# Kernel tuning notes

Hardware: AMD Instinct MI355X
Metric: run time of the kernel (lower is better)

The kernel has to match this reference:

```python
import jax, jax.numpy as jnp
import numpy as np

H_PARAM = 3.0   # filtering strength h
TWS = 5         # template window size
SWS = 11        # search window size


def _shift_stack(x, window_size):
    # [N,C,H,W] -> [N,C,H,W,window_size**2] of circularly shifted copies.
    # Shift order matches the torch module: outer loop x_shift, inner y_shift,
    # roll shifts=(y_shift, x_shift) on dims (H, W).
    r = window_size // 2
    return jnp.stack(
        [jnp.roll(x, (ys, xs), axis=(2, 3))
         for xs in range(-r, r + 1) for ys in range(-r, r + 1)],
        axis=-1,
    )


def _box_filter(x, window_size):
    # Circular box-sum over H,W dims. The torch double roll loop is separable,
    # so do it as two 1-D roll sums (10 rolls instead of 25 for tws=5).
    r = window_size // 2
    s = x
    acc = x
    for k in range(1, r + 1):
        acc = acc + jnp.roll(s, k, axis=3) + jnp.roll(s, -k, axis=3)
    s2 = acc
    for k in range(1, r + 1):
        acc = acc + jnp.roll(s2, k, axis=2) + jnp.roll(s2, -k, axis=2)
    return acc


def setup_inputs() -> dict:
    key = jax.random.key(0)
    x = jax.random.uniform(key, (2, 3, 512, 512), dtype=jnp.float32)
    return {"x": x}


def reference(x):
    # luminance (RGB input: C == 3)
    xc = jnp.clip(x, 0.0, 1.0)
    y = 0.299 * xc[:, :1] + 0.587 * xc[:, 1:2] + 0.114 * xc[:, 2:3]  # [N,1,H,W]

    x_stack = _shift_stack(x, SWS)  # [N,3,H,W,sws^2]
    y_stack = _shift_stack(y, SWS)  # [N,1,H,W,sws^2]

    d2 = _box_filter((y[..., None] - y_stack) ** 2, TWS)  # [N,1,H,W,sws^2]
    distances = jnp.sqrt(d2)
    weights = jnp.exp(-distances / H_PARAM)                # [N,1,H,W,sws^2]

    denoised = (weights * x_stack).sum(axis=-1) / weights.sum(axis=-1)
    return jnp.clip(denoised, 0.0, 1.0)
```

## Files before the change

kernel.cpp:

```cpp
#include <hip/hip_runtime.h>
#include <math.h>


#define H_IMG 512
#define W_IMG 512
#define MASK  511
#define HWSZ  (H_IMG * W_IMG)
#define TILE  32
#define HALO  7
#define XD    46
#define YSTR  48
#define HSTR  44
#define VSTR  44

typedef _Float16 h2 __attribute__((ext_vector_type(2)));

__device__ __forceinline__ float fdot2(h2 a, h2 b, float c) {
#if __has_builtin(__builtin_amdgcn_fdot2)
    return __builtin_amdgcn_fdot2(a, b, c, false);
#else
    return c + (float)a.x * (float)b.x + (float)a.y * (float)b.y;
#endif
}

__device__ __forceinline__ float fast_exp2(float x) {
#if __has_builtin(__builtin_amdgcn_exp2f)
    return __builtin_amdgcn_exp2f(x);
#else
    return __expf(x * 0.6931471805599453f);
#endif
}

#define K2C   0.23126321070979063f
#define N2K2 -0.46252642141958126f

__global__ __launch_bounds__(256, 4)
void nlm_kernel(const float* __restrict__ x, float* __restrict__ out) {
    __shared__ float4   ldsX[XD * XD];
    __shared__ float    ldsYf[XD * YSTR];
    __shared__ unsigned ldsY2[XD * YSTR];
    __shared__ float    ldsH[XD * HSTR];
    __shared__ float    ldsV[42 * VSTR];

    const int n  = blockIdx.z;
    const int ti = blockIdx.y * TILE;
    const int tj = blockIdx.x * TILE;
    const int tx = threadIdx.x;
    const int ty = threadIdx.y;
    const int tid = ty * 32 + tx;

    const float* xb = x + (size_t)n * 3 * HWSZ;

    for (int e = tid; e < XD * XD; e += 256) {
        int r = e / XD, c = e - r * XD;
        int gi = (ti + r - HALO) & MASK;
        int gj = (tj + c - HALO) & MASK;
        size_t o = (size_t)gi * W_IMG + gj;
        ldsX[e] = make_float4(xb[o], xb[o + HWSZ], xb[o + 2 * HWSZ], 0.f);
    }
    __syncthreads();

    for (int e = tid; e < XD * 47; e += 256) {
        int r = e / 47, c = e - r * 47;
        int cs = (c == 46) ? 45 : c;
        float4 v = ldsX[r * XD + cs];
        float rr = fminf(fmaxf(v.x, 0.f), 1.f);
        float gg = fminf(fmaxf(v.y, 0.f), 1.f);
        float bb = fminf(fmaxf(v.z, 0.f), 1.f);
        ldsYf[r * YSTR + c] = 0.299f * rr + 0.587f * gg + 0.114f * bb;
    }
    __syncthreads();

    for (int e = tid; e < XD * XD; e += 256) {
        int r = e / XD, c = e - r * XD;
        h2 p;
        p.x = (_Float16)ldsYf[r * YSTR + c];
        p.y = (_Float16)ldsYf[r * YSTR + c + 1];
        ldsY2[r * YSTR + c] = __builtin_bit_cast(unsigned, p);
    }
    __syncthreads();

    for (int e = tid; e < XD * 42; e += 256) {
        int r = e / 42, c = e - r * 42;
        h2 a  = __builtin_bit_cast(h2, ldsY2[r * YSTR + c]);
        h2 b  = __builtin_bit_cast(h2, ldsY2[r * YSTR + c + 2]);
        h2 cc = __builtin_bit_cast(h2, ldsY2[r * YSTR + c + 4]);
        float x0 = (float)a.x, x1 = (float)a.y;
        float x2 = (float)b.x, x3 = (float)b.y;
        float x4 = (float)cc.x;
        ldsH[r * HSTR + c] = x0*x0 + x1*x1 + x2*x2 + x3*x3 + x4*x4;
    }
    __syncthreads();

    for (int e = tid; e < 42 * 42; e += 256) {
        int r = e / 42, c = e - r * 42;
        const float* hp = &ldsH[r * HSTR + c];
        float s = ((hp[0] + hp[HSTR]) + (hp[2*HSTR] + hp[3*HSTR])) + hp[4*HSTR];
        ldsV[r * VSTR + c] = K2C * s;
    }
    __syncthreads();

    const int jl = tx + HALO;
    const int il = ty * 4 + HALO;

    h2 cyP[8][3];
    float Vc[4];
    {
        float hcv[8];
        #pragma unroll
        for (int t = 0; t < 8; ++t) {
            int base = (il - 2 + t) * YSTR + (jl - 2);
            cyP[t][0] = __builtin_bit_cast(h2, ldsY2[base]);
            cyP[t][1] = __builtin_bit_cast(h2, ldsY2[base + 2]);
            h2 z = __builtin_bit_cast(h2, ldsY2[base + 4]);
            z.y = (_Float16)0.f;
            cyP[t][2] = z;
            hcv[t] = ldsH[(il - 2 + t) * HSTR + (jl - 2)];
        }
        float v0 = ((hcv[0] + hcv[1]) + (hcv[2] + hcv[3])) + hcv[4];
        float v1 = v0 - hcv[0] + hcv[5];
        float v2 = v1 - hcv[1] + hcv[6];
        float v3 = v2 - hcv[2] + hcv[7];
        Vc[0] = K2C * v0; Vc[1] = K2C * v1; Vc[2] = K2C * v2; Vc[3] = K2C * v3;
    }

    float den[4]  = {0.f, 0.f, 0.f, 0.f};
    float num0[4] = {0.f, 0.f, 0.f, 0.f};
    float num1[4] = {0.f, 0.f, 0.f, 0.f};
    float num2[4] = {0.f, 0.f, 0.f, 0.f};

    #pragma unroll 1
    for (int xs = -5; xs <= 5; ++xs) {
        const int jc  = jl - xs - 2;
        const int xjc = jl - xs;

        h2     swP[8][3];
        float  Wr[4];
        float4 xw[4];

        #pragma unroll
        for (int t = 0; t < 8; ++t) {
            int base = (il - 7 + t) * YSTR + jc;
            swP[t][0] = __builtin_bit_cast(h2, ldsY2[base]);
            swP[t][1] = __builtin_bit_cast(h2, ldsY2[base + 2]);
            swP[t][2] = __builtin_bit_cast(h2, ldsY2[base + 4]);
        }
        #pragma unroll
        for (int t = 0; t < 4; ++t) {
            Wr[t] = ldsV[(il - 7 + t) * VSTR + jc];
            xw[t] = ldsX[(il - 5 + t) * XD + xjc];
        }

        #pragma unroll
        for (int k = 0; k <= 10; ++k) {
            h2 nsw0, nsw1, nsw2; float nWv; float4 nxw;
            if (k < 10) {
                const int nr = il + k + 1;
                int base = nr * YSTR + jc;
                nsw0 = __builtin_bit_cast(h2, ldsY2[base]);
                nsw1 = __builtin_bit_cast(h2, ldsY2[base + 2]);
                nsw2 = __builtin_bit_cast(h2, ldsY2[base + 4]);
                nWv  = ldsV[(il + k - 3) * VSTR + jc];
                nxw  = ldsX[(il + k - 1) * XD + xjc];
            }

            float s[8];
            #pragma unroll
            for (int t = 0; t < 8; ++t) {
                const int m = (t + k) & 7;
                s[t] = fdot2(cyP[t][0], swP[m][0],
                       fdot2(cyP[t][1], swP[m][1],
                       fdot2(cyP[t][2], swP[m][2], 0.f)));
            }

            float S0 = ((s[0] + s[1]) + (s[2] + s[3])) + s[4];
            float S1 = S0 - s[0] + s[5];
            float S2 = S1 - s[1] + s[6];
            float S3 = S2 - s[2] + s[7];

            float d2a[4];
            d2a[0] = fmaf(N2K2, S0, Vc[0] + Wr[k & 3]);
            d2a[1] = fmaf(N2K2, S1, Vc[1] + Wr[(k + 1) & 3]);
            d2a[2] = fmaf(N2K2, S2, Vc[2] + Wr[(k + 2) & 3]);
            d2a[3] = fmaf(N2K2, S3, Vc[3] + Wr[(k + 3) & 3]);

            #pragma unroll
            for (int o = 0; o < 4; ++o) {
                float sd = __builtin_amdgcn_sqrtf(__builtin_fabsf(d2a[o]));
                float w  = fast_exp2(-sd);
                float4 xv = xw[(k + o) & 3];
                num0[o] = fmaf(w, xv.x, num0[o]);
                num1[o] = fmaf(w, xv.y, num1[o]);
                num2[o] = fmaf(w, xv.z, num2[o]);
                den[o] += w;
            }

            if (k < 10) {
                swP[k & 7][0] = nsw0;
                swP[k & 7][1] = nsw1;
                swP[k & 7][2] = nsw2;
                Wr[k & 3] = nWv;
                xw[k & 3] = nxw;
            }
        }
    }

    float* ob = out + (size_t)n * 3 * HWSZ;
    #pragma unroll
    for (int o = 0; o < 4; ++o) {
        int gi = ti + ty * 4 + o;
        int gj = tj + tx;
        size_t off = (size_t)gi * W_IMG + gj;
        float inv = __builtin_amdgcn_rcpf(den[o]);
        float v0 = fminf(fmaxf(num0[o] * inv, 0.f), 1.f);
        float v1 = fminf(fmaxf(num1[o] * inv, 0.f), 1.f);
        float v2 = fminf(fmaxf(num2[o] * inv, 0.f), 1.f);
        ob[off]            = v0;
        ob[off + HWSZ]     = v1;
        ob[off + 2 * HWSZ] = v2;
    }
}

extern "C" void kernel_launch(void* const* d_in, const int* in_sizes, int n_in,
                              void* d_out, int out_size, void* d_ws, size_t ws_size,
                              hipStream_t stream) {
    const float* x = (const float*)d_in[0];
    float* out = (float*)d_out;
    dim3 grid(W_IMG / TILE, H_IMG / TILE, 2);
    dim3 block(32, 8);
    nlm_kernel<<<grid, block, 0, stream>>>(x, out);
}
```

Measured before the change: 98.98 us.

## Double threads per tile, each computing two output rows instead of four

Raises the block to 512 threads (32x16) and cuts each thread's register-blocked strip from four rows to two, shrinking the sliding window of template rows from 8 to 6. Centre V values now come from the precomputed ldsV table. The aim is more parallelism per tile and lower register pressure. The cost is less reuse of the sliding window: each thread handles 6 template rows for 2 outputs instead of 8 for 4, so dot-product work and LDS loads per output pixel go up.

```diff
diff --git a/kernel.cpp b/kernel.cpp
--- a/kernel.cpp
+++ b/kernel.cpp
@@ -12,6 +12,7 @@
 #define YSTR  48
 #define HSTR  44
 #define VSTR  44
+#define NTHR  512
 
 typedef _Float16 h2 __attribute__((ext_vector_type(2)));
 
@@ -34,7 +35,7 @@
 #define K2C   0.23126321070979063f
 #define N2K2 -0.46252642141958126f
 
-__global__ __launch_bounds__(256, 4)
+__global__ __launch_bounds__(NTHR, 4)
 void nlm_kernel(const float* __restrict__ x, float* __restrict__ out) {
     __shared__ float4   ldsX[XD * XD];
     __shared__ float    ldsYf[XD * YSTR];
@@ -51,7 +52,7 @@
 
     const float* xb = x + (size_t)n * 3 * HWSZ;
 
-    for (int e = tid; e < XD * XD; e += 256) {
+    for (int e = tid; e < XD * XD; e += NTHR) {
         int r = e / XD, c = e - r * XD;
         int gi = (ti + r - HALO) & MASK;
         int gj = (tj + c - HALO) & MASK;
@@ -60,7 +61,7 @@
     }
     __syncthreads();
 
-    for (int e = tid; e < XD * 47; e += 256) {
+    for (int e = tid; e < XD * 47; e += NTHR) {
         int r = e / 47, c = e - r * 47;
         int cs = (c == 46) ? 45 : c;
         float4 v = ldsX[r * XD + cs];
@@ -71,7 +72,7 @@
     }
     __syncthreads();
 
-    for (int e = tid; e < XD * XD; e += 256) {
+    for (int e = tid; e < XD * XD; e += NTHR) {
         int r = e / XD, c = e - r * XD;
         h2 p;
         p.x = (_Float16)ldsYf[r * YSTR + c];
@@ -80,7 +81,7 @@
     }
     __syncthreads();
 
-    for (int e = tid; e < XD * 42; e += 256) {
+    for (int e = tid; e < XD * 42; e += NTHR) {
         int r = e / 42, c = e - r * 42;
         h2 a  = __builtin_bit_cast(h2, ldsY2[r * YSTR + c]);
         h2 b  = __builtin_bit_cast(h2, ldsY2[r * YSTR + c + 2]);
@@ -92,7 +93,7 @@
     }
     __syncthreads();
 
-    for (int e = tid; e < 42 * 42; e += 256) {
+    for (int e = tid; e < 42 * 42; e += NTHR) {
         int r = e / 42, c = e - r * 42;
         const float* hp = &ldsH[r * HSTR + c];
         float s = ((hp[0] + hp[HSTR]) + (hp[2*HSTR] + hp[3*HSTR])) + hp[4*HSTR];
@@ -101,73 +102,64 @@
     __syncthreads();
 
     const int jl = tx + HALO;
-    const int il = ty * 4 + HALO;
-
-    h2 cyP[8][3];
-    float Vc[4];
-    {
-        float hcv[8];
-        #pragma unroll
-        for (int t = 0; t < 8; ++t) {
-            int base = (il - 2 + t) * YSTR + (jl - 2);
-            cyP[t][0] = __builtin_bit_cast(h2, ldsY2[base]);
-            cyP[t][1] = __builtin_bit_cast(h2, ldsY2[base + 2]);
-            h2 z = __builtin_bit_cast(h2, ldsY2[base + 4]);
-            z.y = (_Float16)0.f;
-            cyP[t][2] = z;
-            hcv[t] = ldsH[(il - 2 + t) * HSTR + (jl - 2)];
-        }
-        float v0 = ((hcv[0] + hcv[1]) + (hcv[2] + hcv[3])) + hcv[4];
-        float v1 = v0 - hcv[0] + hcv[5];
-        float v2 = v1 - hcv[1] + hcv[6];
-        float v3 = v2 - hcv[2] + hcv[7];
-        Vc[0] = K2C * v0; Vc[1] = K2C * v1; Vc[2] = K2C * v2; Vc[3] = K2C * v3;
-    }
-
-    float den[4]  = {0.f, 0.f, 0.f, 0.f};
-    float num0[4] = {0.f, 0.f, 0.f, 0.f};
-    float num1[4] = {0.f, 0.f, 0.f, 0.f};
-    float num2[4] = {0.f, 0.f, 0.f, 0.f};
+    const int il = ty * 2 + HALO;
+
+    h2 cyP[6][3];
+    float Vc[2];
+    #pragma unroll
+    for (int t = 0; t < 6; ++t) {
+        int base = (il - 2 + t) * YSTR + (jl - 2);
+        cyP[t][0] = __builtin_bit_cast(h2, ldsY2[base]);
+        cyP[t][1] = __builtin_bit_cast(h2, ldsY2[base + 2]);
+        h2 z = __builtin_bit_cast(h2, ldsY2[base + 4]);
+        z.y = (_Float16)0.f;
+        cyP[t][2] = z;
+    }
+    Vc[0] = ldsV[(il - 2) * VSTR + (jl - 2)];
+    Vc[1] = ldsV[(il - 1) * VSTR + (jl - 2)];
+
+    float den[2]  = {0.f, 0.f};
+    float num0[2] = {0.f, 0.f};
+    float num1[2] = {0.f, 0.f};
+    float num2[2] = {0.f, 0.f};
 
     #pragma unroll 1
     for (int xs = -5; xs <= 5; ++xs) {
         const int jc  = jl - xs - 2;
         const int xjc = jl - xs;
 
-        h2     swP[8][3];
-        float  Wr[4];
-        float4 xw[4];
+        h2     swP[6][3];
+        float  Wr[2];
+        float4 xw[2];
 
         #pragma unroll
-        for (int t = 0; t < 8; ++t) {
+        for (int t = 0; t < 6; ++t) {
             int base = (il - 7 + t) * YSTR + jc;
             swP[t][0] = __builtin_bit_cast(h2, ldsY2[base]);
             swP[t][1] = __builtin_bit_cast(h2, ldsY2[base + 2]);
             swP[t][2] = __builtin_bit_cast(h2, ldsY2[base + 4]);
         }
-        #pragma unroll
-        for (int t = 0; t < 4; ++t) {
-            Wr[t] = ldsV[(il - 7 + t) * VSTR + jc];
-            xw[t] = ldsX[(il - 5 + t) * XD + xjc];
-        }
+        Wr[0] = ldsV[(il - 7) * VSTR + jc];
+        Wr[1] = ldsV[(il - 6) * VSTR + jc];
+        xw[0] = ldsX[(il - 5) * XD + xjc];
+        xw[1] = ldsX[(il - 4) * XD + xjc];
 
         #pragma unroll
         for (int k = 0; k <= 10; ++k) {
             h2 nsw0, nsw1, nsw2; float nWv; float4 nxw;
             if (k < 10) {
-                const int nr = il + k + 1;
-                int base = nr * YSTR + jc;
+                int base = (il + k - 1) * YSTR + jc;
                 nsw0 = __builtin_bit_cast(h2, ldsY2[base]);
                 nsw1 = __builtin_bit_cast(h2, ldsY2[base + 2]);
                 nsw2 = __builtin_bit_cast(h2, ldsY2[base + 4]);
-                nWv  = ldsV[(il + k - 3) * VSTR + jc];
-                nxw  = ldsX[(il + k - 1) * XD + xjc];
-            }
-
-            float s[8];
+                nWv  = ldsV[(il + k - 5) * VSTR + jc];
+                nxw  = ldsX[(il + k - 3) * XD + xjc];
+            }
+
+            float s[6];
             #pragma unroll
-            for (int t = 0; t < 8; ++t) {
-                const int m = (t + k) & 7;
+            for (int t = 0; t < 6; ++t) {
+                const int m = (t + k) % 6;
                 s[t] = fdot2(cyP[t][0], swP[m][0],
                        fdot2(cyP[t][1], swP[m][1],
                        fdot2(cyP[t][2], swP[m][2], 0.f)));
@@ -175,40 +167,43 @@
 
             float S0 = ((s[0] + s[1]) + (s[2] + s[3])) + s[4];
             float S1 = S0 - s[0] + s[5];
-            float S2 = S1 - s[1] + s[6];
-            float S3 = S2 - s[2] + s[7];
-
-            float d2a[4];
-            d2a[0] = fmaf(N2K2, S0, Vc[0] + Wr[k & 3]);
-            d2a[1] = fmaf(N2K2, S1, Vc[1] + Wr[(k + 1) & 3]);
-            d2a[2] = fmaf(N2K2, S2, Vc[2] + Wr[(k + 2) & 3]);
-            d2a[3] = fmaf(N2K2, S3, Vc[3] + Wr[(k + 3) & 3]);
-
-            #pragma unroll
-            for (int o = 0; o < 4; ++o) {
-                float sd = __builtin_amdgcn_sqrtf(__builtin_fabsf(d2a[o]));
+
+            float d2a0 = fmaf(N2K2, S0, Vc[0] + Wr[k & 1]);
+            float d2a1 = fmaf(N2K2, S1, Vc[1] + Wr[(k + 1) & 1]);
+
+            {
+                float sd = __builtin_amdgcn_sqrtf(__builtin_fabsf(d2a0));
                 float w  = fast_exp2(-sd);
-                float4 xv = xw[(k + o) & 3];
-                num0[o] = fmaf(w, xv.x, num0[o]);
-                num1[o] = fmaf(w, xv.y, num1[o]);
-                num2[o] = fmaf(w, xv.z, num2[o]);
-                den[o] += w;
+                float4 xv = xw[k & 1];
+                num0[0] = fmaf(w, xv.x, num0[0]);
+                num1[0] = fmaf(w, xv.y, num1[0]);
+                num2[0] = fmaf(w, xv.z, num2[0]);
+                den[0] += w;
+            }
+            {
+                float sd = __builtin_amdgcn_sqrtf(__builtin_fabsf(d2a1));
+                float w  = fast_exp2(-sd);
+                float4 xv = xw[(k + 1) & 1];
+                num0[1] = fmaf(w, xv.x, num0[1]);
+                num1[1] = fmaf(w, xv.y, num1[1]);
+                num2[1] = fmaf(w, xv.z, num2[1]);
+                den[1] += w;
             }
 
             if (k < 10) {
-                swP[k & 7][0] = nsw0;
-                swP[k & 7][1] = nsw1;
-                swP[k & 7][2] = nsw2;
-                Wr[k & 3] = nWv;
-                xw[k & 3] = nxw;
+                swP[k % 6][0] = nsw0;
+                swP[k % 6][1] = nsw1;
+                swP[k % 6][2] = nsw2;
+                Wr[k & 1] = nWv;
+                xw[k & 1] = nxw;
             }
         }
     }
 
     float* ob = out + (size_t)n * 3 * HWSZ;
     #pragma unroll
-    for (int o = 0; o < 4; ++o) {
-        int gi = ti + ty * 4 + o;
+    for (int o = 0; o < 2; ++o) {
+        int gi = ti + ty * 2 + o;
         int gj = tj + tx;
         size_t off = (size_t)gi * W_IMG + gj;
         float inv = __builtin_amdgcn_rcpf(den[o]);
@@ -227,6 +222,6 @@
     const float* x = (const float*)d_in[0];
     float* out = (float*)d_out;
     dim3 grid(W_IMG / TILE, H_IMG / TILE, 2);
-    dim3 block(32, 8);
+    dim3 block(32, 16);
     nlm_kernel<<<grid, block, 0, stream>>>(x, out);
 }
```

After: 105.3 us. +6.4%, slower.

## Software-pipeline weight evaluation, pack FMA accumulators, read center V from LDS

Applied to the files above, without the earlier changes.

The sqrt/exp weight computation and the accumulation for each row are deferred by one iteration of the inner k loop, so the transcendental work overlaps with the next row's dot products and LDS loads. The first two color accumulators are packed into a float2 so the compiler can emit packed FMA. The center-window V terms are now read directly from the precomputed ldsV instead of being rebuilt from ldsH. Launch bounds drop from 4 to 2 blocks per SM, which gives the extra pipelined live values more registers but may reduce occupancy.

```diff
diff --git a/kernel.cpp b/kernel.cpp
--- a/kernel.cpp
+++ b/kernel.cpp
@@ -14,6 +14,7 @@
 #define VSTR  44
 
 typedef _Float16 h2 __attribute__((ext_vector_type(2)));
+typedef float f32x2 __attribute__((ext_vector_type(2)));
 
 __device__ __forceinline__ float fdot2(h2 a, h2 b, float c) {
 #if __has_builtin(__builtin_amdgcn_fdot2)
@@ -34,7 +35,7 @@
 #define K2C   0.23126321070979063f
 #define N2K2 -0.46252642141958126f
 
-__global__ __launch_bounds__(256, 4)
+__global__ __launch_bounds__(256, 2)
 void nlm_kernel(const float* __restrict__ x, float* __restrict__ out) {
     __shared__ float4   ldsX[XD * XD];
     __shared__ float    ldsYf[XD * YSTR];
@@ -105,29 +106,26 @@
 
     h2 cyP[8][3];
     float Vc[4];
-    {
-        float hcv[8];
-        #pragma unroll
-        for (int t = 0; t < 8; ++t) {
-            int base = (il - 2 + t) * YSTR + (jl - 2);
-            cyP[t][0] = __builtin_bit_cast(h2, ldsY2[base]);
-            cyP[t][1] = __builtin_bit_cast(h2, ldsY2[base + 2]);
-            h2 z = __builtin_bit_cast(h2, ldsY2[base + 4]);
-            z.y = (_Float16)0.f;
-            cyP[t][2] = z;
-            hcv[t] = ldsH[(il - 2 + t) * HSTR + (jl - 2)];
-        }
-        float v0 = ((hcv[0] + hcv[1]) + (hcv[2] + hcv[3])) + hcv[4];
-        float v1 = v0 - hcv[0] + hcv[5];
-        float v2 = v1 - hcv[1] + hcv[6];
-        float v3 = v2 - hcv[2] + hcv[7];
-        Vc[0] = K2C * v0; Vc[1] = K2C * v1; Vc[2] = K2C * v2; Vc[3] = K2C * v3;
-    }
-
-    float den[4]  = {0.f, 0.f, 0.f, 0.f};
-    float num0[4] = {0.f, 0.f, 0.f, 0.f};
-    float num1[4] = {0.f, 0.f, 0.f, 0.f};
-    float num2[4] = {0.f, 0.f, 0.f, 0.f};
+    #pragma unroll
+    for (int t = 0; t < 8; ++t) {
+        int base = (il - 2 + t) * YSTR + (jl - 2);
+        cyP[t][0] = __builtin_bit_cast(h2, ldsY2[base]);
+        cyP[t][1] = __builtin_bit_cast(h2, ldsY2[base + 2]);
+        h2 z = __builtin_bit_cast(h2, ldsY2[base + 4]);
+        z.y = (_Float16)0.f;
+        cyP[t][2] = z;
+    }
+    #pragma unroll
+    for (int o = 0; o < 4; ++o)
+        Vc[o] = ldsV[(il - 2 + o) * VSTR + (jl - 2)];
+
+    f32x2 acc01[4];
+    float num2[4], den[4];
+    #pragma unroll
+    for (int o = 0; o < 4; ++o) {
+        acc01[o] = (f32x2){0.f, 0.f};
+        num2[o] = 0.f; den[o] = 0.f;
+    }
 
     #pragma unroll 1
     for (int xs = -5; xs <= 5; ++xs) {
@@ -150,6 +148,9 @@
             Wr[t] = ldsV[(il - 7 + t) * VSTR + jc];
             xw[t] = ldsX[(il - 5 + t) * XD + xjc];
         }
+
+        float  pd2[4];
+        float4 pxv;
 
         #pragma unroll
         for (int k = 0; k <= 10; ++k) {
@@ -184,18 +185,24 @@
             d2a[2] = fmaf(N2K2, S2, Vc[2] + Wr[(k + 2) & 3]);
             d2a[3] = fmaf(N2K2, S3, Vc[3] + Wr[(k + 3) & 3]);
 
+            if (k > 0) {
+                #pragma unroll
+                for (int o = 0; o < 4; ++o) {
+                    float4 xv = (o == 0) ? pxv : xw[(k - 1 + o) & 3];
+                    float sd = __builtin_amdgcn_sqrtf(__builtin_fabsf(pd2[o]));
+                    float w  = fast_exp2(-sd);
+                    f32x2 bw = {w, w};
+                    f32x2 xv01 = {xv.x, xv.y};
+                    acc01[o] = __builtin_elementwise_fma(bw, xv01, acc01[o]);
+                    num2[o] = fmaf(w, xv.z, num2[o]);
+                    den[o] += w;
+                }
+            }
+
             #pragma unroll
-            for (int o = 0; o < 4; ++o) {
-                float sd = __builtin_amdgcn_sqrtf(__builtin_fabsf(d2a[o]));
-                float w  = fast_exp2(-sd);
-                float4 xv = xw[(k + o) & 3];
-                num0[o] = fmaf(w, xv.x, num0[o]);
-                num1[o] = fmaf(w, xv.y, num1[o]);
-                num2[o] = fmaf(w, xv.z, num2[o]);
-                den[o] += w;
-            }
-
+            for (int o = 0; o < 4; ++o) pd2[o] = d2a[o];
             if (k < 10) {
+                pxv = xw[k & 3];
                 swP[k & 7][0] = nsw0;
                 swP[k & 7][1] = nsw1;
                 swP[k & 7][2] = nsw2;
@@ -203,6 +210,18 @@
                 xw[k & 3] = nxw;
             }
         }
+
+        #pragma unroll
+        for (int o = 0; o < 4; ++o) {
+            float4 xv = xw[(10 + o) & 3];
+            float sd = __builtin_amdgcn_sqrtf(__builtin_fabsf(pd2[o]));
+            float w  = fast_exp2(-sd);
+            f32x2 bw = {w, w};
+            f32x2 xv01 = {xv.x, xv.y};
+            acc01[o] = __builtin_elementwise_fma(bw, xv01, acc01[o]);
+            num2[o] = fmaf(w, xv.z, num2[o]);
+            den[o] += w;
+        }
     }
 
     float* ob = out + (size_t)n * 3 * HWSZ;
@@ -212,9 +231,9 @@
         int gj = tj + tx;
         size_t off = (size_t)gi * W_IMG + gj;
         float inv = __builtin_amdgcn_rcpf(den[o]);
-        float v0 = fminf(fmaxf(num0[o] * inv, 0.f), 1.f);
-        float v1 = fminf(fmaxf(num1[o] * inv, 0.f), 1.f);
-        float v2 = fminf(fmaxf(num2[o] * inv, 0.f), 1.f);
+        float v0 = fminf(fmaxf(acc01[o].x * inv, 0.f), 1.f);
+        float v1 = fminf(fmaxf(acc01[o].y * inv, 0.f), 1.f);
+        float v2 = fminf(fmaxf(num2[o]   * inv, 0.f), 1.f);
         ob[off]            = v0;
         ob[off + HWSZ]     = v1;
         ob[off + 2 * HWSZ] = v2;
```

After: 98.42 us. No clear change (-0.6%).

## Process two horizontal shifts per iteration and trade occupancy for ILP

Applied to the files above, without the earlier changes.

Restructures the 11-step horizontal shift loop into one single-shift group followed by five groups that each handle two shifts, interleaving their dot products and exp/sqrt chains to expose more instruction-level parallelism. Launch bounds drop from 4 to 2 waves per SIMD hint so the doubled register state fits. Vc is now read from the precomputed ldsV instead of being recomputed from ldsH. The risk is lower occupancy and register pressure or spills in exchange for fewer loop-carried dependencies.

```diff
diff --git a/kernel.cpp b/kernel.cpp
--- a/kernel.cpp
+++ b/kernel.cpp
@@ -34,7 +34,104 @@
 #define K2C   0.23126321070979063f
 #define N2K2 -0.46252642141958126f
 
-__global__ __launch_bounds__(256, 4)
+template <int NU>
+__device__ __forceinline__ void nlm_xs_group(
+    int xs0, int jl, int il,
+    const unsigned* __restrict__ ldsY2,
+    const float*    __restrict__ ldsV,
+    const float4*   __restrict__ ldsX,
+    const h2 (&cyP)[8][3], const float (&Vc)[4],
+    float (&num0)[4], float (&num1)[4], float (&num2)[4], float (&den)[4])
+{
+    h2     swP[NU][8][3];
+    float  Wr[NU][4];
+    float4 xw[NU][4];
+    int    jc[NU], xjc[NU];
+
+    #pragma unroll
+    for (int u = 0; u < NU; ++u) {
+        const int xs = xs0 + u;
+        jc[u]  = jl - xs - 2;
+        xjc[u] = jl - xs;
+        #pragma unroll
+        for (int t = 0; t < 8; ++t) {
+            int base = (il - 7 + t) * YSTR + jc[u];
+            swP[u][t][0] = __builtin_bit_cast(h2, ldsY2[base]);
+            swP[u][t][1] = __builtin_bit_cast(h2, ldsY2[base + 2]);
+            swP[u][t][2] = __builtin_bit_cast(h2, ldsY2[base + 4]);
+        }
+        #pragma unroll
+        for (int t = 0; t < 4; ++t) {
+            Wr[u][t] = ldsV[(il - 7 + t) * VSTR + jc[u]];
+            xw[u][t] = ldsX[(il - 5 + t) * XD + xjc[u]];
+        }
+    }
+
+    #pragma unroll
+    for (int k = 0; k <= 10; ++k) {
+        h2 nsw[NU][3]; float nWv[NU]; float4 nxw[NU];
+        if (k < 10) {
+            #pragma unroll
+            for (int u = 0; u < NU; ++u) {
+                int base = (il + k + 1) * YSTR + jc[u];
+                nsw[u][0] = __builtin_bit_cast(h2, ldsY2[base]);
+                nsw[u][1] = __builtin_bit_cast(h2, ldsY2[base + 2]);
+                nsw[u][2] = __builtin_bit_cast(h2, ldsY2[base + 4]);
+                nWv[u] = ldsV[(il + k - 3) * VSTR + jc[u]];
+                nxw[u] = ldsX[(il + k - 1) * XD + xjc[u]];
+            }
+        }
+
+        float s[NU][8];
+        #pragma unroll
+        for (int t = 0; t < 8; ++t) {
+            const int m = (t + k) & 7;
+            #pragma unroll
+            for (int u = 0; u < NU; ++u)
+                s[u][t] = fdot2(cyP[t][0], swP[u][m][0],
+                          fdot2(cyP[t][1], swP[u][m][1],
+                          fdot2(cyP[t][2], swP[u][m][2], 0.f)));
+        }
+
+        #pragma unroll
+        for (int u = 0; u < NU; ++u) {
+            float S0 = ((s[u][0] + s[u][1]) + (s[u][2] + s[u][3])) + s[u][4];
+            float S1 = S0 - s[u][0] + s[u][5];
+            float S2 = S1 - s[u][1] + s[u][6];
+            float S3 = S2 - s[u][2] + s[u][7];
+
+            float d2a[4];
+            d2a[0] = fmaf(N2K2, S0, Vc[0] + Wr[u][k & 3]);
+            d2a[1] = fmaf(N2K2, S1, Vc[1] + Wr[u][(k + 1) & 3]);
+            d2a[2] = fmaf(N2K2, S2, Vc[2] + Wr[u][(k + 2) & 3]);
+            d2a[3] = fmaf(N2K2, S3, Vc[3] + Wr[u][(k + 3) & 3]);
+
+            #pragma unroll
+            for (int o = 0; o < 4; ++o) {
+                float sd = __builtin_amdgcn_sqrtf(__builtin_fabsf(d2a[o]));
+                float w  = fast_exp2(-sd);
+                float4 xv = xw[u][(k + o) & 3];
+                num0[o] = fmaf(w, xv.x, num0[o]);
+                num1[o] = fmaf(w, xv.y, num1[o]);
+                num2[o] = fmaf(w, xv.z, num2[o]);
+                den[o] += w;
+            }
+        }
+
+        if (k < 10) {
+            #pragma unroll
+            for (int u = 0; u < NU; ++u) {
+                swP[u][k & 7][0] = nsw[u][0];
+                swP[u][k & 7][1] = nsw[u][1];
+                swP[u][k & 7][2] = nsw[u][2];
+                Wr[u][k & 3] = nWv[u];
+                xw[u][k & 3] = nxw[u];
+            }
+        }
+    }
+}
+
+__global__ __launch_bounds__(256, 2)
 void nlm_kernel(const float* __restrict__ x, float* __restrict__ out) {
     __shared__ float4   ldsX[XD * XD];
     __shared__ float    ldsYf[XD * YSTR];
@@ -105,105 +202,30 @@
 
     h2 cyP[8][3];
     float Vc[4];
-    {
-        float hcv[8];
-        #pragma unroll
-        for (int t = 0; t < 8; ++t) {
-            int base = (il - 2 + t) * YSTR + (jl - 2);
-            cyP[t][0] = __builtin_bit_cast(h2, ldsY2[base]);
-            cyP[t][1] = __builtin_bit_cast(h2, ldsY2[base + 2]);
-            h2 z = __builtin_bit_cast(h2, ldsY2[base + 4]);
-            z.y = (_Float16)0.f;
-            cyP[t][2] = z;
-            hcv[t] = ldsH[(il - 2 + t) * HSTR + (jl - 2)];
-        }
-        float v0 = ((hcv[0] + hcv[1]) + (hcv[2] + hcv[3])) + hcv[4];
-        float v1 = v0 - hcv[0] + hcv[5];
-        float v2 = v1 - hcv[1] + hcv[6];
-        float v3 = v2 - hcv[2] + hcv[7];
-        Vc[0] = K2C * v0; Vc[1] = K2C * v1; Vc[2] = K2C * v2; Vc[3] = K2C * v3;
-    }
-
-    float den[4]  = {0.f, 0.f, 0.f, 0.f};
+    #pragma unroll
+    for (int t = 0; t < 8; ++t) {
+        int base = (il - 2 + t) * YSTR + (jl - 2);
+        cyP[t][0] = __builtin_bit_cast(h2, ldsY2[base]);
+        cyP[t][1] = __builtin_bit_cast(h2, ldsY2[base + 2]);
+        h2 z = __builtin_bit_cast(h2, ldsY2[base + 4]);
+        z.y = (_Float16)0.f;
+        cyP[t][2] = z;
+    }
+    #pragma unroll
+    for (int o = 0; o < 4; ++o)
+        Vc[o] = ldsV[(il - 2 + o) * VSTR + (jl - 2)];
+
     float num0[4] = {0.f, 0.f, 0.f, 0.f};
     float num1[4] = {0.f, 0.f, 0.f, 0.f};
     float num2[4] = {0.f, 0.f, 0.f, 0.f};
-
+    float den[4]  = {0.f, 0.f, 0.f, 0.f};
+
+    nlm_xs_group<1>(-5, jl, il, ldsY2, ldsV, ldsX, cyP, Vc,
+                    num0, num1, num2, den);
     #pragma unroll 1
-    for (int xs = -5; xs <= 5; ++xs) {
-        const int jc  = jl - xs - 2;
-        const int xjc = jl - xs;
-
-        h2     swP[8][3];
-        float  Wr[4];
-        float4 xw[4];
-
-        #pragma unroll
-        for (int t = 0; t < 8; ++t) {
-            int base = (il - 7 + t) * YSTR + jc;
-            swP[t][0] = __builtin_bit_cast(h2, ldsY2[base]);
-            swP[t][1] = __builtin_bit_cast(h2, ldsY2[base + 2]);
-            swP[t][2] = __builtin_bit_cast(h2, ldsY2[base + 4]);
-        }
-        #pragma unroll
-        for (int t = 0; t < 4; ++t) {
-            Wr[t] = ldsV[(il - 7 + t) * VSTR + jc];
-            xw[t] = ldsX[(il - 5 + t) * XD + xjc];
-        }
-
-        #pragma unroll
-        for (int k = 0; k <= 10; ++k) {
-            h2 nsw0, nsw1, nsw2; float nWv; float4 nxw;
-            if (k < 10) {
-                const int nr = il + k + 1;
-                int base = nr * YSTR + jc;
-                nsw0 = __builtin_bit_cast(h2, ldsY2[base]);
-                nsw1 = __builtin_bit_cast(h2, ldsY2[base + 2]);
-                nsw2 = __builtin_bit_cast(h2, ldsY2[base + 4]);
-                nWv  = ldsV[(il + k - 3) * VSTR + jc];
-                nxw  = ldsX[(il + k - 1) * XD + xjc];
-            }
-
-            float s[8];
-            #pragma unroll
-            for (int t = 0; t < 8; ++t) {
-                const int m = (t + k) & 7;
-                s[t] = fdot2(cyP[t][0], swP[m][0],
-                       fdot2(cyP[t][1], swP[m][1],
-                       fdot2(cyP[t][2], swP[m][2], 0.f)));
-            }
-
-            float S0 = ((s[0] + s[1]) + (s[2] + s[3])) + s[4];
-            float S1 = S0 - s[0] + s[5];
-            float S2 = S1 - s[1] + s[6];
-            float S3 = S2 - s[2] + s[7];
-
-            float d2a[4];
-            d2a[0] = fmaf(N2K2, S0, Vc[0] + Wr[k & 3]);
-            d2a[1] = fmaf(N2K2, S1, Vc[1] + Wr[(k + 1) & 3]);
-            d2a[2] = fmaf(N2K2, S2, Vc[2] + Wr[(k + 2) & 3]);
-            d2a[3] = fmaf(N2K2, S3, Vc[3] + Wr[(k + 3) & 3]);
-
-            #pragma unroll
-            for (int o = 0; o < 4; ++o) {
-                float sd = __builtin_amdgcn_sqrtf(__builtin_fabsf(d2a[o]));
-                float w  = fast_exp2(-sd);
-                float4 xv = xw[(k + o) & 3];
-                num0[o] = fmaf(w, xv.x, num0[o]);
-                num1[o] = fmaf(w, xv.y, num1[o]);
-                num2[o] = fmaf(w, xv.z, num2[o]);
-                den[o] += w;
-            }
-
-            if (k < 10) {
-                swP[k & 7][0] = nsw0;
-                swP[k & 7][1] = nsw1;
-                swP[k & 7][2] = nsw2;
-                Wr[k & 3] = nWv;
-                xw[k & 3] = nxw;
-            }
-        }
-    }
+    for (int xp = -4; xp <= 4; xp += 2)
+        nlm_xs_group<2>(xp, jl, il, ldsY2, ldsV, ldsX, cyP, Vc,
+                        num0, num1, num2, den);
 
     float* ob = out + (size_t)n * 3 * HWSZ;
     #pragma unroll
```

Result: slower. 107.6 us (+8.7%).
